# Kernel optimization log

Measured on AMD Instinct MI355X. Metric: run time of the kernel, lower is better.

The kernel has to match this reference:

```python
import jax, jax.numpy as jnp
import numpy as np

EPS = 1e-5  # BatchNorm1d eps


def _glorot(key, shape):
    fan_in, fan_out = shape[0], shape[1]
    lim = float(np.sqrt(6.0 / (fan_in + fan_out)))
    return jax.random.uniform(key, shape, jnp.float32, -lim, lim)


def setup_inputs() -> dict:
    key = jax.random.key(0)
    ks = jax.random.split(key, 6)
    N, IN, H, OUT = 50000, 128, 64, 64
    E = 800000
    x = jax.random.normal(ks[0], (N, IN), jnp.float32)
    edge_index = jax.random.randint(ks[1], (2, E), 0, N, jnp.int64)
    return {
        "x": x,
        "edge_index": edge_index,
        "W1": _glorot(ks[2], (IN, H)),
        "b1": jnp.zeros((H,), jnp.float32),
        "gamma1": jnp.ones((H,), jnp.float32),
        "beta1": jnp.zeros((H,), jnp.float32),
        "W2": _glorot(ks[3], (H, OUT)),
        "b2": jnp.zeros((OUT,), jnp.float32),
        "gamma2": jnp.ones((OUT,), jnp.float32),
        "beta2": jnp.zeros((OUT,), jnp.float32),
    }


def _gcn_conv(x, W, b, src, dst, norm, n):
    # x' = D^{-1/2} (A + I) D^{-1/2} X W + b  (PyG GCNConv, edge_weight=None)
    h = x @ W                              # [N, F]
    msg = h[src] * norm[:, None]           # gather + scale, [E+N, F]
    out = jax.ops.segment_sum(msg, dst, num_segments=n)  # scatter-add
    return out + b


def _batch_norm(h, gamma, beta):
    # training-mode BN over node dim, biased variance (as torch uses for normalization)
    mean = h.mean(0)
    var = h.var(0)
    return (h - mean) * jax.lax.rsqrt(var + EPS) * gamma + beta


def reference(x, edge_index, W1, b1, gamma1, beta1, W2, b2, gamma2, beta2):
    n = x.shape[0]
    # add self loops
    loop = jnp.arange(n, dtype=edge_index.dtype)
    src = jnp.concatenate([edge_index[0], loop])
    dst = jnp.concatenate([edge_index[1], loop])
    # symmetric degree normalization (deg >= 1 thanks to self loops)
    deg = jax.ops.segment_sum(jnp.ones(src.shape[0], x.dtype), dst, num_segments=n)
    dinv = jax.lax.rsqrt(jnp.maximum(deg, 1e-12))
    norm = dinv[src] * dinv[dst]           # [E+N]

    # layer 1: GCNConv -> BN -> ReLU (dropout = identity in eval)
    h = _gcn_conv(x, W1, b1, src, dst, norm, n)
    h = jax.nn.relu(_batch_norm(h, gamma1, beta1))
    # layer 2: GCNConv -> BN (no activation on last layer)
    h = _gcn_conv(h, W2, b2, src, dst, norm, n)
    h = _batch_norm(h, gamma2, beta2)
    return h
```

## Files before the change

### kernel.cpp

```cpp
#include <hip/hip_runtime.h>
#include <hip/hip_fp16.h>
#include <math.h>

#define EPS 1e-5f
#define CAP 64

typedef float v4f __attribute__((ext_vector_type(4)));
typedef unsigned int u32x4 __attribute__((ext_vector_type(4)));
typedef _Float16 half8 __attribute__((ext_vector_type(8)));
typedef float f32x4 __attribute__((ext_vector_type(4)));

__device__ __forceinline__ float xor32sum(float a) {
    return a + __shfl_xor(a, 32, 64);
}

__global__ void k_init(int* __restrict__ cnt, float* __restrict__ stats,
                       __half* __restrict__ Ylo, __half* __restrict__ Yhi, int N) {
    int i = blockIdx.x * blockDim.x + threadIdx.x;
    if (i < N) cnt[i] = 0;
    if (i < 256) stats[i] = 0.0f;
    if (i < 16) {
        ((int*)(Ylo + (size_t)N * 32))[i] = 0;
        ((int*)(Yhi + (size_t)N * 32))[i] = 0;
    }
}

__global__ __launch_bounds__(256) void k_gemm1_fill(const float* __restrict__ x,
                                                    const float* __restrict__ W1,
                                                    __half* __restrict__ Ylo,
                                                    __half* __restrict__ Yhi, int N,
                                                    const int* __restrict__ src,
                                                    const int* __restrict__ dst,
                                                    int* __restrict__ cnt,
                                                    unsigned short* __restrict__ csr,
                                                    int E, int G) {
    if ((int)blockIdx.x >= G) {
        int t = (blockIdx.x - G) * 256 + threadIdx.x;
        int stride = (gridDim.x - G) * 256;
        for (int e = t; e < E; e += stride) {
            int d = dst[e];
            int pos = atomicAdd(&cnt[d], 1);
            if (pos < CAP)
                __builtin_nontemporal_store((unsigned short)src[e], &csr[(size_t)d * CAP + pos]);
        }
        return;
    }
    int lane = threadIdx.x & 63;
    int wave = threadIdx.x >> 6;
    int ln15 = lane & 15;
    int kg = lane >> 4;
    half8 Bf[4][4];
#pragma unroll
    for (int kt = 0; kt < 4; ++kt)
#pragma unroll
        for (int ct = 0; ct < 4; ++ct) {
            half8 b;
#pragma unroll
            for (int j = 0; j < 8; ++j)
                b[j] = (_Float16)W1[(size_t)(kt * 32 + kg * 8 + j) * 64 + ct * 16 + ln15];
            Bf[kt][ct] = b;
        }
    int nrb = (N + 15) >> 4;
    int gw = blockIdx.x * 4 + wave;
    int nwv = G * 4;
    for (int rb = gw; rb < nrb; rb += nwv) {
        int row = min(rb * 16 + ln15, N - 1);
        const float4* xr = (const float4*)(x + (size_t)row * 128);
        f32x4 acc[4];
#pragma unroll
        for (int ct = 0; ct < 4; ++ct) acc[ct] = (f32x4){0.f, 0.f, 0.f, 0.f};
#pragma unroll
        for (int kt = 0; kt < 4; ++kt) {
            float4 v0 = xr[kt * 8 + kg * 2];
            float4 v1 = xr[kt * 8 + kg * 2 + 1];
            half8 A;
            A[0] = (_Float16)v0.x; A[1] = (_Float16)v0.y;
            A[2] = (_Float16)v0.z; A[3] = (_Float16)v0.w;
            A[4] = (_Float16)v1.x; A[5] = (_Float16)v1.y;
            A[6] = (_Float16)v1.z; A[7] = (_Float16)v1.w;
#pragma unroll
            for (int ct = 0; ct < 4; ++ct)
                acc[ct] = __builtin_amdgcn_mfma_f32_16x16x32_f16(A, Bf[kt][ct], acc[ct], 0, 0, 0);
        }
#pragma unroll
        for (int ct = 0; ct < 4; ++ct) {
            int col = ct * 16 + ln15;
            __half* Yo = (col >= 32) ? Yhi : Ylo;
            int cc = col & 31;
#pragma unroll
            for (int i = 0; i < 4; ++i) {
                int gr = rb * 16 + kg * 4 + i;
                if (gr < N) Yo[(size_t)gr * 32 + cc] = __float2half(acc[ct][i]);
            }
        }
    }
}

__global__ void k_scale(const int* __restrict__ cnt, float* __restrict__ dinv,
                        __half* __restrict__ Ylo, __half* __restrict__ Yhi, int N) {
    int i = blockIdx.x * blockDim.x + threadIdx.x;
    if (i == 0) dinv[N] = 0.0f;
    int row = i >> 2, c4 = i & 3;
    if (row >= N) return;
    float dv = rsqrtf((float)(cnt[row] + 1));
    if (c4 == 0) dinv[row] = dv;
    union U16 { uint4 u; __half2 h[4]; } t;
#pragma unroll
    for (int buf = 0; buf < 2; ++buf) {
        __half* Y = buf ? Yhi : Ylo;
        uint4* p = (uint4*)(Y + (size_t)row * 32 + c4 * 8);
        t.u = *p;
#pragma unroll
        for (int k = 0; k < 4; ++k) {
            float2 f = __half22float2(t.h[k]);
            t.h[k] = __float22half2_rn(make_float2(f.x * dv, f.y * dv));
        }
        *p = t.u;
    }
}

template <bool HALF_OUT>
__global__ __launch_bounds__(256) void k_agg(const __half* __restrict__ Ylo,
                                             const __half* __restrict__ Yhi,
                                             const unsigned short* __restrict__ csr,
                                             const int* __restrict__ cnt,
                                             const float* __restrict__ dinv,
                                             void* __restrict__ Hout,
                                             float* __restrict__ stats, int N) {
    __shared__ float ssum[4][32], ssq[4][32];
    int half = blockIdx.x & 1;
    const __half* Y = half ? Yhi : Ylo;
    int lane = threadIdx.x & 63;
    int wave = threadIdx.x >> 6;
    int fl = lane & 3;
    int node = (lane >> 2) & 3;
    int g = lane >> 4;
    int gd = g >> 1;
    int gsh = (g & 1) << 4;
    float selfmask = (g == 0) ? 1.f : 0.f;
    int slot = (blockIdx.x >> 1) * 4 + wave;
    int nslots = (gridDim.x >> 1) * 4;
    float s[8], q[8];
#pragma unroll
    for (int j = 0; j < 8; ++j) { s[j] = 0.f; q[j] = 0.f; }
    union U16 { uint4 u; __half2 h[4]; };
    for (int base = slot * 4; base < N; base += nslots * 4) {
        int myv = base + node;
        bool vok = myv < N;
        int vs = vok ? myv : N;
        int c  = vok ? min(cnt[myv], CAP) : 0;
        float dv = dinv[vs];
        const unsigned int* crow =
            (const unsigned int*)(csr + (size_t)(vok ? myv : 0) * CAP);
        float a[8];
        {
            U16 t; t.u = *(const uint4*)(Y + (size_t)vs * 32 + fl * 8);
#pragma unroll
            for (int k = 0; k < 4; ++k) {
                float2 f = __half22float2(t.h[k]);
                a[2 * k]     = selfmask * f.x;
                a[2 * k + 1] = selfmask * f.y;
            }
        }
        for (int b = 0; b < 16; ++b) {
            if (__all(4 * b >= c)) break;
            unsigned int w = crow[2 * b + gd];
            bool live = vok && (4 * b + g < c);
            int ent = live ? (int)((w >> gsh) & 0xFFFFu) : 0xFFFF;
            int idx = min(ent, N);
            U16 t; t.u = *(const uint4*)(Y + (size_t)idx * 32 + fl * 8);
#pragma unroll
            for (int k = 0; k < 4; ++k) {
                float2 f = __half22float2(t.h[k]);
                a[2 * k]     += f.x;
                a[2 * k + 1] += f.y;
            }
        }
#pragma unroll
        for (int j = 0; j < 8; ++j) {
            a[j] += __shfl_xor(a[j], 16, 64);
            a[j] = xor32sum(a[j]) * dv;
        }
        if (g == 0 && vok) {
            if (HALF_OUT) {
                __half* H1 = (__half*)Hout;
                union { u32x4 u; __half2 h[4]; } o;
#pragma unroll
                for (int k = 0; k < 4; ++k)
                    o.h[k] = __floats2half2_rn(a[2 * k], a[2 * k + 1]);
                __builtin_nontemporal_store(o.u,
                    (u32x4*)(H1 + (size_t)myv * 64 + half * 32 + fl * 8));
            } else {
                float* H = (float*)Hout;
                v4f lo = {a[0], a[1], a[2], a[3]};
                v4f hi = {a[4], a[5], a[6], a[7]};
                float* dst = H + (size_t)myv * 64 + half * 32 + fl * 8;
                __builtin_nontemporal_store(lo, (v4f*)dst);
                __builtin_nontemporal_store(hi, (v4f*)(dst + 4));
            }
        }
#pragma unroll
        for (int j = 0; j < 8; ++j) { s[j] += a[j]; q[j] += a[j] * a[j]; }
    }
#pragma unroll
    for (int j = 0; j < 8; ++j) {
        s[j] += __shfl_xor(s[j], 4, 64); s[j] += __shfl_xor(s[j], 8, 64);
        q[j] += __shfl_xor(q[j], 4, 64); q[j] += __shfl_xor(q[j], 8, 64);
    }
    if (lane < 4) {
#pragma unroll
        for (int j = 0; j < 8; ++j) {
            ssum[wave][fl * 8 + j] = s[j];
            ssq[wave][fl * 8 + j]  = q[j];
        }
    }
    __syncthreads();
    if (threadIdx.x < 32) {
        float ts = ssum[0][threadIdx.x] + ssum[1][threadIdx.x] + ssum[2][threadIdx.x] + ssum[3][threadIdx.x];
        float tq = ssq[0][threadIdx.x] + ssq[1][threadIdx.x] + ssq[2][threadIdx.x] + ssq[3][threadIdx.x];
        atomicAdd(&stats[half * 32 + threadIdx.x], ts);
        atomicAdd(&stats[64 + half * 32 + threadIdx.x], tq);
    }
}

__global__ __launch_bounds__(256) void k_gemm2(const __half* __restrict__ H1,
                                               const float* __restrict__ stats,
                                               const float* __restrict__ gamma,
                                               const float* __restrict__ beta,
                                               const float* __restrict__ W2,
                                               const float* __restrict__ dinv,
                                               __half* __restrict__ Ylo,
                                               __half* __restrict__ Yhi, int N) {
    int lane = threadIdx.x & 63;
    int wave = threadIdx.x >> 6;
    int ln15 = lane & 15;
    int kg = lane >> 4;
    float sc[2][8], sh[2][8];
#pragma unroll
    for (int kt = 0; kt < 2; ++kt)
#pragma unroll
        for (int j = 0; j < 8; ++j) {
            int k = kt * 32 + kg * 8 + j;
            float mean = stats[k] / (float)N;
            float var = stats[64 + k] / (float)N - mean * mean;
            float s = rsqrtf(var + EPS) * gamma[k];
            sc[kt][j] = s;
            sh[kt][j] = beta[k] - mean * s;
        }
    half8 Bf[2][4];
#pragma unroll
    for (int kt = 0; kt < 2; ++kt)
#pragma unroll
        for (int ct = 0; ct < 4; ++ct) {
            half8 b;
#pragma unroll
            for (int j = 0; j < 8; ++j)
                b[j] = (_Float16)W2[(size_t)(kt * 32 + kg * 8 + j) * 64 + ct * 16 + ln15];
            Bf[kt][ct] = b;
        }
    int nrb = (N + 15) >> 4;
    int gw = blockIdx.x * 4 + wave;
    int nwv = gridDim.x * 4;
    for (int rb = gw; rb < nrb; rb += nwv) {
        int row = min(rb * 16 + ln15, N - 1);
        const __half* hr = H1 + (size_t)row * 64;
        f32x4 acc[4];
#pragma unroll
        for (int ct = 0; ct < 4; ++ct) acc[ct] = (f32x4){0.f, 0.f, 0.f, 0.f};
#pragma unroll
        for (int kt = 0; kt < 2; ++kt) {
            union { uint4 u; __half h[8]; } t;
            t.u = *(const uint4*)(hr + kt * 32 + kg * 8);
            half8 A;
#pragma unroll
            for (int j = 0; j < 8; ++j) {
                float v = __half2float(t.h[j]);
                v = fmaxf(v * sc[kt][j] + sh[kt][j], 0.f);
                A[j] = (_Float16)v;
            }
#pragma unroll
            for (int ct = 0; ct < 4; ++ct)
                acc[ct] = __builtin_amdgcn_mfma_f32_16x16x32_f16(A, Bf[kt][ct], acc[ct], 0, 0, 0);
        }
        float4 dv4 = *(const float4*)(dinv + rb * 16 + kg * 4);
#pragma unroll
        for (int ct = 0; ct < 4; ++ct) {
            int col = ct * 16 + ln15;
            __half* Yo = (col >= 32) ? Yhi : Ylo;
            int cc = col & 31;
#pragma unroll
            for (int i = 0; i < 4; ++i) {
                int gr = rb * 16 + kg * 4 + i;
                float dvv = (i == 0) ? dv4.x : (i == 1) ? dv4.y : (i == 2) ? dv4.z : dv4.w;
                if (gr < N) Yo[(size_t)gr * 32 + cc] = __float2half(acc[ct][i] * dvv);
            }
        }
    }
}

__global__ void k_bnfinal(float* __restrict__ out, const float* __restrict__ stats,
                          const float* __restrict__ gamma, const float* __restrict__ beta,
                          int N) {
    int i = blockIdx.x * blockDim.x + threadIdx.x;
    int total = N * 64;
    if (i < total) {
        int f = i & 63;
        float mean = stats[f] / (float)N;
        float var = stats[64 + f] / (float)N - mean * mean;
        float rstd = rsqrtf(var + EPS);
        out[i] = (out[i] - mean) * rstd * gamma[f] + beta[f];
    }
}

extern "C" void kernel_launch(void* const* d_in, const int* in_sizes, int n_in,
                              void* d_out, int out_size, void* d_ws, size_t ws_size,
                              hipStream_t stream) {
    const float* x      = (const float*)d_in[0];
    const int*   ei     = (const int*)d_in[1];
    const float* W1     = (const float*)d_in[2];
    const float* gamma1 = (const float*)d_in[4];
    const float* beta1  = (const float*)d_in[5];
    const float* W2     = (const float*)d_in[6];
    const float* gamma2 = (const float*)d_in[8];
    const float* beta2  = (const float*)d_in[9];
    float* out = (float*)d_out;

    const int N = in_sizes[0] / 128;
    const int E = in_sizes[1] / 2;
    const int* src = ei;
    const int* dst = ei + E;

    char* ws = (char*)d_ws;
    int*   cnt   = (int*)  ws;
    float* stats = (float*)(ws + 0x40000);
    float* dinv  = (float*)(ws + 0x50000);
    __half* Ylo  = (__half*)(ws + 0x90000);
    __half* Yhi  = (__half*)(ws + 0x90000 + 0x320000);
    __half* H1   = (__half*)(ws + 0x90000 + 0x640000);
    unsigned short* csr = (unsigned short*)(ws + 0x90000 + 0x640000 + 0xC40000);

    const int B = (N + 255) / 256;
    const int total = N * 64;
    const int G = 768, F = 256;

    k_init<<<B, 256, 0, stream>>>(cnt, stats, Ylo, Yhi, N);

    k_gemm1_fill<<<G + F, 256, 0, stream>>>(x, W1, Ylo, Yhi, N, src, dst, cnt, csr, E, G);
    k_scale<<<(N * 4 + 255) / 256, 256, 0, stream>>>(cnt, dinv, Ylo, Yhi, N);
    k_agg<true><<<1250, 256, 0, stream>>>(Ylo, Yhi, csr, cnt, dinv, H1, stats, N);

    k_gemm2<<<784, 256, 0, stream>>>(H1, stats, gamma1, beta1, W2, dinv, Ylo, Yhi, N);
    k_agg<false><<<1250, 256, 0, stream>>>(Ylo, Yhi, csr, cnt, dinv, out, stats + 128, N);
    k_bnfinal<<<(total + 255) / 256, 256, 0, stream>>>(out, stats + 128, gamma2, beta2, N);
}
```

Measured before the change: 244.5 us.

## Build CSR via two-level bucketed counting sort instead of global atomics

Replaces the global atomicAdd-per-edge CSR fill with a counting sort. A shared-memory histogram over 256-node buckets is built alongside GEMM1, followed by a single-block scan, a per-block scatter into bucketed bins, and a per-bucket kernel that builds each bucket's CSR slice in LDS and writes it out coalesced. Degree scaling is fused into the CSR build, which removes k_scale and the global cnt zeroing. The aim is to avoid scattered global atomics and random 2-byte stores, at the cost of three extra launches, a serial one-block scan, and only 64 blocks doing the scatter.

```diff
diff --git a/kernel.cpp b/kernel.cpp
--- a/kernel.cpp
+++ b/kernel.cpp
@@ -14,35 +14,34 @@
     return a + __shfl_xor(a, 32, 64);
 }
 
-__global__ void k_init(int* __restrict__ cnt, float* __restrict__ stats,
+__global__ void k_init(float* __restrict__ stats, float* __restrict__ dinv,
                        __half* __restrict__ Ylo, __half* __restrict__ Yhi, int N) {
-    int i = blockIdx.x * blockDim.x + threadIdx.x;
-    if (i < N) cnt[i] = 0;
+    int i = threadIdx.x;
     if (i < 256) stats[i] = 0.0f;
     if (i < 16) {
         ((int*)(Ylo + (size_t)N * 32))[i] = 0;
         ((int*)(Yhi + (size_t)N * 32))[i] = 0;
     }
-}
-
-__global__ __launch_bounds__(256) void k_gemm1_fill(const float* __restrict__ x,
+    if (i == 0) dinv[N] = 0.0f;
+}
+
+__global__ __launch_bounds__(256) void k_gemm1_hist(const float* __restrict__ x,
                                                     const float* __restrict__ W1,
                                                     __half* __restrict__ Ylo,
                                                     __half* __restrict__ Yhi, int N,
-                                                    const int* __restrict__ src,
                                                     const int* __restrict__ dst,
-                                                    int* __restrict__ cnt,
-                                                    unsigned short* __restrict__ csr,
+                                                    int* __restrict__ hist,
                                                     int E, int G) {
     if ((int)blockIdx.x >= G) {
-        int t = (blockIdx.x - G) * 256 + threadIdx.x;
-        int stride = (gridDim.x - G) * 256;
-        for (int e = t; e < E; e += stride) {
-            int d = dst[e];
-            int pos = atomicAdd(&cnt[d], 1);
-            if (pos < CAP)
-                __builtin_nontemporal_store((unsigned short)src[e], &csr[(size_t)d * CAP + pos]);
-        }
+        __shared__ int h[256];
+        int b = blockIdx.x - G;
+        h[threadIdx.x] = 0;
+        __syncthreads();
+        long long e0 = (long long)E * b / 64, e1 = (long long)E * (b + 1) / 64;
+        for (int e = (int)e0 + (int)threadIdx.x; e < (int)e1; e += 256)
+            atomicAdd(&h[dst[e] >> 8], 1);
+        __syncthreads();
+        hist[b * 256 + threadIdx.x] = h[threadIdx.x];
         return;
     }
     int lane = threadIdx.x & 63;
@@ -96,26 +95,108 @@
     }
 }
 
-__global__ void k_scale(const int* __restrict__ cnt, float* __restrict__ dinv,
-                        __half* __restrict__ Ylo, __half* __restrict__ Yhi, int N) {
-    int i = blockIdx.x * blockDim.x + threadIdx.x;
-    if (i == 0) dinv[N] = 0.0f;
-    int row = i >> 2, c4 = i & 3;
-    if (row >= N) return;
-    float dv = rsqrtf((float)(cnt[row] + 1));
-    if (c4 == 0) dinv[row] = dv;
-    union U16 { uint4 u; __half2 h[4]; } t;
-#pragma unroll
-    for (int buf = 0; buf < 2; ++buf) {
-        __half* Y = buf ? Yhi : Ylo;
-        uint4* p = (uint4*)(Y + (size_t)row * 32 + c4 * 8);
-        t.u = *p;
+__global__ void k_scan(const int* __restrict__ hist, int* __restrict__ off, int NB) {
+    __shared__ int sh[256];
+    int j = threadIdx.x;
+    int tot = 0;
+    for (int b = 0; b < 64; ++b) tot += (j < NB) ? hist[b * 256 + j] : 0;
+    int p16 = (tot + 15) & ~15;
+    sh[j] = p16;
+    __syncthreads();
+    for (int o = 1; o < 256; o <<= 1) {
+        int t = (j >= o) ? sh[j - o] : 0;
+        __syncthreads();
+        sh[j] += t;
+        __syncthreads();
+    }
+    int s = sh[j] - p16;
+    for (int b = 0; b < 64; ++b) {
+        if (j < NB) {
+            off[b * 256 + j] = s;
+            s += hist[b * 256 + j];
+        }
+    }
+}
+
+__global__ void k_binscatter(const int* __restrict__ src, const int* __restrict__ dst,
+                             const int* __restrict__ off, unsigned int* __restrict__ bin,
+                             int E) {
+    __shared__ int cur[256];
+    int b = blockIdx.x;
+    cur[threadIdx.x] = off[b * 256 + threadIdx.x];
+    __syncthreads();
+    long long e0 = (long long)E * b / 64, e1 = (long long)E * (b + 1) / 64;
+    for (int e = (int)e0 + (int)threadIdx.x; e < (int)e1; e += 256) {
+        int d = dst[e], s = src[e];
+        int pos = atomicAdd(&cur[d >> 8], 1);
+        unsigned int probe = bin[pos];
+        asm volatile("" :: "v"(probe));
+        bin[pos] = ((unsigned)(d & 255) << 16) | (unsigned)s;
+    }
+}
+
+__global__ __launch_bounds__(256) void k_csrbuild(const unsigned int* __restrict__ bin,
+                                                  const int* __restrict__ hist,
+                                                  const int* __restrict__ off,
+                                                  unsigned short* __restrict__ csr,
+                                                  int* __restrict__ cnt,
+                                                  float* __restrict__ dinv,
+                                                  __half* __restrict__ Ylo,
+                                                  __half* __restrict__ Yhi, int N) {
+    __shared__ unsigned short lcsr[256 * CAP];
+    __shared__ int lcnt[256];
+    __shared__ float ldv[256];
+    int tid = threadIdx.x, j0 = blockIdx.x;
+    lcnt[tid] = 0;
+    __syncthreads();
+    for (int b = 0; b < 64; ++b) {
+        int start = off[b * 256 + j0], len = hist[b * 256 + j0];
+        for (int i = tid; i < len; i += 256) {
+            unsigned v = bin[start + i];
+            int node = v >> 16, s = v & 0xFFFF;
+            int p = atomicAdd(&lcnt[node], 1);
+            if (p < CAP) lcsr[node * CAP + p] = (unsigned short)s;
+        }
+    }
+    __syncthreads();
+    uint4* gp = (uint4*)(csr + (size_t)j0 * 256 * CAP);
+    const uint4* lp = (const uint4*)lcsr;
+    for (int i = tid; i < 2048; i += 256) gp[i] = lp[i];
+    int g = j0 * 256 + tid;
+    float dv = 0.f;
+    if (g < N) {
+        int c = lcnt[tid];
+        cnt[g] = c;
+        dv = rsqrtf((float)(c + 1));
+        dinv[g] = dv;
+    }
+    ldv[tid] = dv;
+    __syncthreads();
+    int nrow = N - j0 * 256;
+    if (nrow > 256) nrow = 256;
+    if (nrow < 0) nrow = 0;
+    int nu4 = nrow * 4;
+    for (int i = tid; i < nu4; i += 256) {
+        int r = i >> 2;
+        float dvv = ldv[r];
+        size_t base = ((size_t)(j0 * 256 + r)) * 32 + (size_t)(i & 3) * 8;
+        union U { uint4 u; __half2 h[4]; } t;
+        uint4* p0 = (uint4*)(Ylo + base);
+        t.u = *p0;
 #pragma unroll
         for (int k = 0; k < 4; ++k) {
             float2 f = __half22float2(t.h[k]);
-            t.h[k] = __float22half2_rn(make_float2(f.x * dv, f.y * dv));
-        }
-        *p = t.u;
+            t.h[k] = __float22half2_rn(make_float2(f.x * dvv, f.y * dvv));
+        }
+        *p0 = t.u;
+        uint4* p1 = (uint4*)(Yhi + base);
+        t.u = *p1;
+#pragma unroll
+        for (int k = 0; k < 4; ++k) {
+            float2 f = __half22float2(t.h[k]);
+            t.h[k] = __float22half2_rn(make_float2(f.x * dvv, f.y * dvv));
+        }
+        *p1 = t.u;
     }
 }
 
@@ -329,24 +410,29 @@
     const int E = in_sizes[1] / 2;
     const int* src = ei;
     const int* dst = ei + E;
+    const int NB = (N + 255) >> 8;
 
     char* ws = (char*)d_ws;
     int*   cnt   = (int*)  ws;
     float* stats = (float*)(ws + 0x40000);
     float* dinv  = (float*)(ws + 0x50000);
     __half* Ylo  = (__half*)(ws + 0x90000);
-    __half* Yhi  = (__half*)(ws + 0x90000 + 0x320000);
-    __half* H1   = (__half*)(ws + 0x90000 + 0x640000);
-    unsigned short* csr = (unsigned short*)(ws + 0x90000 + 0x640000 + 0xC40000);
-
-    const int B = (N + 255) / 256;
+    __half* Yhi  = (__half*)(ws + 0x3B0000);
+    __half* H1   = (__half*)(ws + 0x6D0000);
+    unsigned short* csr = (unsigned short*)(ws + 0xD10000);
+    unsigned int* bin   = (unsigned int*)(ws + 0x1340000);
+    int* hist    = (int*)(ws + 0x1690000);
+    int* off     = (int*)(ws + 0x16A0000);
+
     const int total = N * 64;
-    const int G = 768, F = 256;
-
-    k_init<<<B, 256, 0, stream>>>(cnt, stats, Ylo, Yhi, N);
-
-    k_gemm1_fill<<<G + F, 256, 0, stream>>>(x, W1, Ylo, Yhi, N, src, dst, cnt, csr, E, G);
-    k_scale<<<(N * 4 + 255) / 256, 256, 0, stream>>>(cnt, dinv, Ylo, Yhi, N);
+    const int G = 768;
+
+    k_init<<<1, 256, 0, stream>>>(stats, dinv, Ylo, Yhi, N);
+
+    k_gemm1_hist<<<G + 64, 256, 0, stream>>>(x, W1, Ylo, Yhi, N, dst, hist, E, G);
+    k_scan<<<1, 256, 0, stream>>>(hist, off, NB);
+    k_binscatter<<<64, 256, 0, stream>>>(src, dst, off, bin, E);
+    k_csrbuild<<<NB, 256, 0, stream>>>(bin, hist, off, csr, cnt, dinv, Ylo, Yhi, N);
     k_agg<true><<<1250, 256, 0, stream>>>(Ylo, Yhi, csr, cnt, dinv, H1, stats, N);
 
     k_gemm2<<<784, 256, 0, stream>>>(H1, stats, gamma1, beta1, W2, dinv, Ylo, Yhi, N);
```

After: 287.7 us. 17.7% more time.
